# Kernel tuning notes

Measured on AMD Instinct MI355X. Metric: run time of the kernel, lower is better.

The kernel has to match this reference:

```python
import jax, jax.numpy as jnp
import numpy as np

NEG = 0.2  # LeakyReLU slope

def lrelu(x):
    return jnp.where(x >= 0, x, NEG * x)

def conv2d(x, w, pad):
    return jax.lax.conv_general_dilated(x, w, (1, 1), [(pad, pad), (pad, pad)],
                                        dimension_numbers=('NCHW', 'OIHW', 'NCHW'))

def maxpool2(x):
    return jax.lax.reduce_window(x, -jnp.inf, jax.lax.max, (1, 1, 2, 2), (1, 1, 2, 2), 'VALID')

def batchnorm(x, g, b, eps=1e-5):
    m = jnp.mean(x, axis=(0, 2, 3), keepdims=True)
    v = jnp.var(x, axis=(0, 2, 3), keepdims=True)
    return (x - m) / jnp.sqrt(v + eps) * g[None, :, None, None] + b[None, :, None, None]

def features(x, cw1, bg1, bb1, cw2, bg2, bb2, cw3, bg3, bb3, cw4, bg4, bb4):
    x = maxpool2(lrelu(batchnorm(conv2d(x, cw1, 1), bg1, bb1)))
    x = maxpool2(lrelu(batchnorm(conv2d(x, cw2, 1), bg2, bb2)))
    x = lrelu(batchnorm(conv2d(x, cw3, 1), bg3, bb3))
    x = lrelu(batchnorm(conv2d(x, cw4, 1), bg4, bb4))
    return x  # [B,64,16,16]

def mhsa(x, wq, bq, wk, bk, wv, bv, rel_h, rel_w, ln_g, ln_b, heads=4):
    B, C, W, H = x.shape
    d, hw = C // heads, W * H
    def proj(w, b):
        return (jnp.einsum('oc,bchw->bohw', w, x) + b[None, :, None, None]).reshape(B, heads, d, hw)
    q, k, v = proj(wq, bq), proj(wk, bk), proj(wv, bv)
    cc = jnp.einsum('bhdi,bhdj->bhij', q, k)                 # content-content
    pos = (rel_h + rel_w).reshape(heads, d, hw)              # relative position bias
    cp = jnp.einsum('hdi,bhdj->bhij', pos, q)                # content-position
    attn = jax.nn.softmax(cc + cp, axis=-1)
    out = jnp.einsum('bhdj,bhij->bhdi', v, attn).reshape(B, C, W, H)
    m = jnp.mean(out, axis=(1, 2, 3), keepdims=True)
    va = jnp.var(out, axis=(1, 2, 3), keepdims=True)
    out = (out - m) / jnp.sqrt(va + 1e-5) * ln_g[None] + ln_b[None]
    return out + x

def cbam(x, cw1, cb1, cw2, cb2, sw, sb):
    avg, mx = jnp.mean(x, axis=(2, 3)), jnp.max(x, axis=(2, 3))
    def exc(f):
        return jnp.einsum('oc,bc->bo', cw2, jax.nn.relu(jnp.einsum('oc,bc->bo', cw1, f) + cb1)) + cb2
    x = jax.nn.sigmoid(exc(avg) + exc(mx))[:, :, None, None] * x
    sf = jnp.stack([jnp.mean(x, axis=1), jnp.max(x, axis=1)], axis=1)  # [B,2,H,W]
    sa = jax.nn.sigmoid(conv2d(sf, sw, 3) + sb[None, :, None, None])
    return sa * x

def sa_module(x, mh, cb):
    return mhsa(x, *mh) + cbam(x, *cb) + x

def setup_inputs() -> dict:
    key = jax.random.key(0)
    ks = jax.random.split(key, 24)
    rn = lambda k, s, sc=1.0: jax.random.normal(k, s, dtype=jnp.float32) * sc
    inp = {
        'input1': rn(ks[0], (64, 1, 64, 64)),
        'input2': rn(ks[1], (5, 5, 1, 64, 64)),
        'conv1_w': rn(ks[2], (64, 1, 3, 3), 0.3),
        'bn1_g': jnp.ones(64), 'bn1_b': jnp.zeros(64),
        'conv2_w': rn(ks[3], (64, 64, 3, 3), 0.05),
        'bn2_g': jnp.ones(64), 'bn2_b': jnp.zeros(64),
        'conv3_w': rn(ks[4], (64, 64, 3, 3), 0.05),
        'bn3_g': jnp.ones(64), 'bn3_b': jnp.zeros(64),
        'conv4_w': rn(ks[5], (64, 64, 3, 3), 0.05),
        'bn4_g': jnp.ones(64), 'bn4_b': jnp.zeros(64),
        'wq': rn(ks[6], (64, 64), 0.12), 'bq': rn(ks[7], (64,), 0.01),
        'wk': rn(ks[8], (64, 64), 0.12), 'bk': rn(ks[9], (64,), 0.01),
        'wv': rn(ks[10], (64, 64), 0.12), 'bv': rn(ks[11], (64,), 0.01),
        'rel_h': rn(ks[12], (1, 4, 16, 1, 16)),
        'rel_w': rn(ks[13], (1, 4, 16, 16, 1)),
        'ln_g': jnp.ones((64, 16, 16)), 'ln_b': jnp.zeros((64, 16, 16)),
        'ca_w1': rn(ks[14], (4, 64), 0.15), 'ca_b1': jnp.zeros(4),
        'ca_w2': rn(ks[15], (64, 4), 0.15), 'ca_b2': jnp.zeros(64),
        'sa_w': rn(ks[16], (1, 2, 7, 7), 0.1), 'sa_b': jnp.zeros(1),
        'cls_w': rn(ks[17], (256,), 0.05),
    }
    return inp

def reference(input1, input2, conv1_w, bn1_g, bn1_b, conv2_w, bn2_g, bn2_b,
              conv3_w, bn3_g, bn3_b, conv4_w, bn4_g, bn4_b,
              wq, bq, wk, bk, wv, bv, rel_h, rel_w, ln_g, ln_b,
              ca_w1, ca_b1, ca_w2, ca_b2, sa_w, sa_b, cls_w):
    fa = (conv1_w, bn1_g, bn1_b, conv2_w, bn2_g, bn2_b, conv3_w, bn3_g, bn3_b, conv4_w, bn4_g, bn4_b)
    mh = (wq, bq, wk, bk, wv, bv, rel_h, rel_w, ln_g, ln_b)
    cb = (ca_w1, ca_b1, ca_w2, ca_b2, sa_w, sa_b)
    q = sa_module(features(input1, *fa), mh, cb)                      # [B,64,16,16]
    S = jax.vmap(lambda imgs: sa_module(features(imgs, *fa), mh, cb))(input2)  # [ncls,shot,64,16,16]
    ncls, shot = input2.shape[0], input2.shape[1]
    B, C, Hh, Ww = q.shape
    hw = Hh * Ww
    # per-class covariance over channels (CovaBlock.cal_covariance)
    X = S.transpose(0, 2, 1, 3, 4).reshape(ncls, C, shot * hw)
    Xc = X - jnp.mean(X, axis=2, keepdims=True)
    cov = jnp.einsum('ncm,ndm->ncd', Xc, Xc) / (hw * shot - 1)        # [ncls,C,C]
    # query similarity: diag(q^T Cov q) done as fused quadratic form
    Q = q.reshape(B, C, hw)
    Qn = Q / jnp.linalg.norm(Q, axis=2, keepdims=True)
    sim = jnp.einsum('bci,jcd,bdi->bji', Qn, cov, Qn)                 # [B,ncls,hw]
    # classifier: LeakyReLU -> Dropout(eval=identity) -> Conv1d(k=hw, stride=hw, no bias)
    out = jnp.einsum('bjk,k->bj', lrelu(sim), cls_w)
    return out
```

## Files before the change

kernel.cpp:

```cpp
#include <hip/hip_runtime.h>
#include <hip/hip_bf16.h>

__device__ __forceinline__ float lrelu(float x){ return x >= 0.f ? x : 0.2f*x; }
__device__ __forceinline__ float sigm(float x){ return 1.f/(1.f+__expf(-x)); }

typedef short short8 __attribute__((ext_vector_type(8)));
typedef float f32x16 __attribute__((ext_vector_type(16)));

static constexpr size_t OFF_X0    = 0;
static constexpr size_t OFF_POS   = 475712;
static constexpr size_t OFF_WQT   = 492096;
static constexpr size_t OFF_STATS = 504384;
static constexpr size_t OFF_P1    = 507456;
static constexpr size_t OFF_P2    = 7092224;
static constexpr size_t OFF_S3    = 8937728;
static constexpr size_t OFF_S4    = 8943872;
static constexpr size_t OFF_WH3   = 8950016;
static constexpr size_t OFF_WL3   = 8968448;
static constexpr size_t OFF_WH4   = 8986880;
static constexpr size_t OFF_WL4   = 9005312;
static constexpr size_t OFF_RES   = 10714688;
static constexpr size_t OFF_MU    = 12172864;
static constexpr size_t OFF_COV   = 12173184;
static constexpr size_t OFF_SIM   = 12193664;
static constexpr size_t OFF_R1    = 12275584;
static constexpr size_t OFF_C2    = OFF_R1;
static constexpr size_t OFF_ATP   = OFF_R1;
static constexpr size_t OFF_C3    = OFF_R1 + 5832704;
static constexpr size_t OFF_C4    = OFF_R1 + 8749056;
static constexpr size_t OFF_CKV   = OFF_R1 + 10207232;
static constexpr size_t OFF_C3P   = OFF_R1 + 10207232;
static constexpr size_t OFF_MHRAW = OFF_R1 + 14581760;
static constexpr size_t OFF_QN    = OFF_R1 + 17543680;
static constexpr size_t OFF_WH    = OFF_R1 + 21737984;
static constexpr size_t OFF_WL    = OFF_WH + 18432;

__device__ __forceinline__ int bn_group(int img){ return (img < 64) ? 0 : (1 + (img-64)/5); }

__device__ __forceinline__ void bn_ab(const float* __restrict__ sums, int g, int c, float n,
                                      float gw, float bw, float& a, float& b)
{
    const float sum = sums[(g*64+c)*2], ss = sums[(g*64+c)*2+1];
    const float m = sum/n;
    const float var = fmaxf(ss/n - m*m, 0.f);
    const float istd = 1.f/sqrtf(var + 1e-5f);
    a = gw*istd;
    b = bw - m*a;
}

__device__ __forceinline__ void bn_ab_s8(const float* __restrict__ sums, int g, int c, float n,
                                         float gw, float bw, float& a, float& b)
{
    float sum = 0.f, ss = 0.f;
#pragma unroll
    for (int s=0;s<8;s++){
        sum += sums[s*768 + (g*64+c)*2];
        ss  += sums[s*768 + (g*64+c)*2 + 1];
    }
    const float m = sum/n;
    const float var = fmaxf(ss/n - m*m, 0.f);
    const float istd = 1.f/sqrtf(var + 1e-5f);
    a = gw*istd;
    b = bw - m*a;
}

__global__ __launch_bounds__(256) void prep_k(const float* __restrict__ in1, const float* __restrict__ in2,
        const float* __restrict__ relh, const float* __restrict__ relw,
        const float* __restrict__ wq, const float* __restrict__ wk, const float* __restrict__ wv,
        const float* __restrict__ cw2, const float* __restrict__ cw3, const float* __restrict__ cw4,
        float* __restrict__ ws)
{
    int idx = blockIdx.x*256 + threadIdx.x;
    if (idx < 364544) { ws[OFF_X0+idx] = (idx < 262144 ? in1[idx] : in2[idx-262144]); return; }
    idx -= 364544;
    if (idx < 16384) {
        const int h = idx>>12, r = idx&4095, i = r>>4, d = r&15;
        ws[OFF_POS+idx] = relh[h*256 + d*16 + (i&15)] + relw[h*256 + d*16 + (i>>4)];
        return;
    }
    idx -= 16384;
    if (idx < 12288) {
        const int s = idx/4096, r = idx%4096, c = r>>6, o = r&63;
        const float* wp = (s==0)?wq:((s==1)?wk:wv);
        ws[OFF_WQT+idx] = wp[o*64 + c];
        return;
    }
    idx -= 12288;
    if (idx < 3072) { ws[OFF_STATS+idx] = 0.f; return; }
    idx -= 3072;
    if (idx < 20480) { ws[OFF_COV+idx] = 0.f; return; }
    idx -= 20480;
    if (idx < 12288) { ws[OFF_S3+idx] = 0.f; return; }
    idx -= 12288;
    if (idx < 110592) {
        const int which = idx / 36864, r0 = idx - which*36864;
        const int och = r0/576, rr = r0%576, cin = rr/9, k9 = rr%9;
        const float* cwp = (which==0)?cw2:((which==1)?cw3:cw4);
        const float v = cwp[r0];
        __hip_bfloat16 hb = __float2bfloat16(v);
        const float hv = __bfloat162float(hb);
        __hip_bfloat16 lb = __float2bfloat16(v - hv);
        const size_t oh = (which==0)?OFF_WH:((which==1)?OFF_WH3:OFF_WH4);
        const size_t ol = (which==0)?OFF_WL:((which==1)?OFF_WL3:OFF_WL4);
        unsigned short* WH = (unsigned short*)(ws + oh);
        unsigned short* WL = (unsigned short*)(ws + ol);
        const int d = k9*4096 + och*64 + cin;
        WH[d] = *(unsigned short*)&hb;
        WL[d] = *(unsigned short*)&lb;
        return;
    }
    idx -= 110592;
    if (idx < 751872) {
        const int img = idx/8448, r = idx%8448;
        const int pos = r>>6, d = r&63;
        int ypad, xpad;
        if (pos < 68){ ypad = (pos<34)?0:33; xpad = (pos<34)?pos:(pos-34); }
        else { const int q = pos-68; ypad = 1 + (q>>1); xpad = (q&1)*33; }
        ws[OFF_P1 + (((size_t)img*34 + ypad)*34 + xpad)*64 + d] = 0.f;
        return;
    }
    idx -= 751872;
    if (idx < 387328) {
        const int img = idx/4352, r = idx%4352;
        const int pos = r>>6, d = r&63;
        int ypad, xpad;
        if (pos < 36){ ypad = (pos<18)?0:17; xpad = (pos<18)?pos:(pos-18); }
        else { const int q = pos-36; ypad = 1 + (q>>1); xpad = (q&1)*17; }
        ws[OFF_P2 + (((size_t)img*18 + ypad)*18 + xpad)*64 + d] = 0.f;
        return;
    }
    idx -= 387328;
    if (idx < 387328) {
        const int img = idx/4352, r = idx%4352;
        const int pos = r>>6, d = r&63;
        int ypad, xpad;
        if (pos < 36){ ypad = (pos<18)?0:17; xpad = (pos<18)?pos:(pos-18); }
        else { const int q = pos-36; ypad = 1 + (q>>1); xpad = (q&1)*17; }
        ws[OFF_C3P + (((size_t)img*18 + ypad)*18 + xpad)*64 + d] = 0.f;
    }
}

template<int H, int W, int CIN, int CH, int OCB, int PT, bool STORE, bool INBN>
__global__ __launch_bounds__(256) void conv3x3_k(const float* __restrict__ in,
                                                 const float* __restrict__ wt,
                                                 float* __restrict__ out,
                                                 float* __restrict__ bnsum,
// ... 152 lines not shown
    }
    const int g = bn_group(img);
    const float n = (float)(((g==0)?64:5) * 4096);
    __syncthreads();
    const int p = t>>1, half = t&1;
    const int ly = p>>5, ox = p&31;
    float r[4][4];
#pragma unroll
    for (int dy=0;dy<4;dy++){
        const float* Lr = xl + (2*ly+dy)*64;
#pragma unroll
        for (int dx=0;dx<4;dx++){
            const int xx = 2*ox-1+dx;
            r[dy][dx] = (xx>=0 && xx<64) ? Lr[xx] : 0.f;
        }
    }
    short8 hv[4], lv[4];
#pragma unroll
    for (int o=0;o<32;o++){
        const int och = half*32 + o;
        float w[9];
#pragma unroll
        for (int k=0;k<9;k++) w[k] = cw[och*9+k];
        float a, b;
        bn_ab(sums, g, och, n, gw[och], bw[och], a, b);
        float best = -1e30f;
#pragma unroll
        for (int sy=0;sy<2;sy++)
#pragma unroll
          for (int sx=0;sx<2;sx++){
            float s=0.f;
#pragma unroll
            for (int ky=0;ky<3;ky++)
#pragma unroll
              for (int kx=0;kx<3;kx++) s += r[sy+ky][sx+kx]*w[ky*3+kx];
            best = fmaxf(best, lrelu(a*s+b));
          }
        __hip_bfloat16 hb = __float2bfloat16(best);
        const float hf = __bfloat162float(hb);
        __hip_bfloat16 lb = __float2bfloat16(best - hf);
        hv[o>>3][o&7] = (short)*(unsigned short*)&hb;
        lv[o>>3][o&7] = (short)*(unsigned short*)&lb;
    }
    const size_t base = ((((size_t)img*34 + (oy0+ly) + 1)*34) + ox + 1)*128 + half*32;
#pragma unroll
    for (int j=0;j<4;j++){
        *(short8*)(p1p + base + j*8)      = hv[j];
        *(short8*)(p1p + base + 64 + j*8) = lv[j];
    }
}

__global__ __launch_bounds__(256) void conv2mfma_k(const unsigned short* __restrict__ p1p,
        const unsigned short* __restrict__ whi, const unsigned short* __restrict__ wlo,
        float* __restrict__ c2)
{
    __shared__ __align__(16) unsigned short Bx[136*128];
    const int img = blockIdx.x, rowblk = blockIdx.y;
    const int t = threadIdx.x;
    {
        const unsigned short* src = p1p + (((size_t)img*34 + rowblk*2)*34)*128;
        for (int idx=t; idx<2176; idx+=256){
            const int pos = idx>>4, sub = idx&15;
            const short8 v = *(const short8*)(src + pos*128 + sub*8);
            *(short8*)(Bx + pos*128 + ((sub ^ (pos&7))<<3)) = v;
        }
    }
    __syncthreads();
    const int lane = t & 63, wv = t >> 6;
    const int mt = wv & 1, ntp = wv >> 1;
    const int m = lane & 31, kg = lane >> 5;
    f32x16 acc;
#pragma unroll
    for (int r=0;r<16;r++) acc[r]=0.f;

#pragma unroll
    for (int ky=0; ky<3; ky++){
#pragma unroll
      for (int kx=0; kx<3; kx++){
        const int s = ky*3 + kx;
        const unsigned short* wh = whi + ((s*64 + mt*32 + m)<<6) + kg*8;
        const unsigned short* wl = wlo + ((s*64 + mt*32 + m)<<6) + kg*8;
        const int pos = (ntp+ky)*34 + m + kx;
        const int pb  = pos << 7;
        const int sw  = (pos & 7) << 3;
#pragma unroll
        for (int ch=0; ch<4; ch++){
            const short8 ah = *(const short8*)(wh + ch*16);
            const short8 al = *(const short8*)(wl + ch*16);
            const short8 bh = *(const short8*)(Bx + pb + ((ch*16 + (kg<<3)) ^ sw));
            const short8 bl = *(const short8*)(Bx + pb + (64 + ((ch*16 + (kg<<3)) ^ sw)));
            acc = __builtin_amdgcn_mfma_f32_32x32x16_bf16(ah, bh, acc, 0,0,0);
            acc = __builtin_amdgcn_mfma_f32_32x32x16_bf16(al, bh, acc, 0,0,0);
            acc = __builtin_amdgcn_mfma_f32_32x32x16_bf16(ah, bl, acc, 0,0,0);
        }
      }
    }
    const int py = rowblk*2 + ntp;
    float* co = c2 + ((size_t)img*64)*1024 + py*32 + m;
#pragma unroll
    for (int r=0; r<16; r++){
        const int och = mt*32 + (r&3) + 8*(r>>2) + 4*kg;
        co[(size_t)och*1024] = acc[r];
    }
}

__global__ __launch_bounds__(256) void bnstats2_k(const float* __restrict__ in, float* __restrict__ sums)
{
    __shared__ float rs[4], rq[4];
    const int img = blockIdx.x, c = blockIdx.y, t = threadIdx.x;
    const float4 v = ((const float4*)(in + ((size_t)img*64 + c)*1024))[t];
    float s = v.x+v.y+v.z+v.w;
    float q = v.x*v.x+v.y*v.y+v.z*v.z+v.w*v.w;
#pragma unroll
    for (int off=32; off>0; off>>=1){ s += __shfl_xor(s, off); q += __shfl_xor(q, off); }
    if ((t&63)==0){ rs[t>>6]=s; rq[t>>6]=q; }
    __syncthreads();
    if (t==0){
        const int g = bn_group(img);
        atomicAdd(&sums[(g*64+c)*2],   rs[0]+rs[1]+rs[2]+rs[3]);
        atomicAdd(&sums[(g*64+c)*2+1], rq[0]+rq[1]+rq[2]+rq[3]);
    }
}

__global__ __launch_bounds__(256) void bnpool_pack_k(const float* __restrict__ c2,
        const float* __restrict__ sums, const float* __restrict__ gw, const float* __restrict__ bw,
        unsigned short* __restrict__ p2p)
{
    __shared__ float aA[64], aB[64];
    const int img = blockIdx.x, cb = blockIdx.y, t = threadIdx.x;
    const int g = bn_group(img);
    if (t < 64){
        const float n = (float)(((g==0)?64:5) * 1024);
        float a, b;
        bn_ab(sums, g, t, n, gw[t], bw[t], a, b);
        aA[t]=a; aB[t]=b;
    }
    __syncthreads();
    const int oy = t>>4, ox = t&15;
    const float* pim = c2 + (size_t)img*65536 + (size_t)cb*32768 + oy*64 + ox*2;
    short8 hv[4], lv[4];
#pragma unroll
    for (int j8=0;j8<4;j8++){
#pragma unroll
      for (int e=0;e<8;e++){
        const int j = j8*8 + e;
        const int c = cb*32 + j;
        const float* pl = pim + (size_t)j*1024;
        const float2 u = *(const float2*)pl;
        const float2 v = *(const float2*)(pl + 32);
        const float a = aA[c], b = aB[c];
        const float best = fmaxf(fmaxf(lrelu(a*u.x+b), lrelu(a*u.y+b)),
                                 fmaxf(lrelu(a*v.x+b), lrelu(a*v.y+b)));
        __hip_bfloat16 hb = __float2bfloat16(best);
        const float hf = __bfloat162float(hb);
        __hip_bfloat16 lb = __float2bfloat16(best - hf);
        hv[j8][e] = (short)*(unsigned short*)&hb;
        lv[j8][e] = (short)*(unsigned short*)&lb;
      }
    }
    unsigned short* dst = p2p + (((size_t)img*18 + oy+1)*18 + ox+1)*128 + cb*32;
#pragma unroll
    for (int j=0;j<4;j++){
        *(short8*)(dst + j*8)      = hv[j];
        *(short8*)(dst + 64 + j*8) = lv[j];
    }
}

__global__ __launch_bounds__(256) void conv16mfma_k(const unsigned short* __restrict__ pack,
        const unsigned short* __restrict__ whi, const unsigned short* __restrict__ wlo,
        float* __restrict__ out, float* __restrict__ bnsum)
{
    __shared__ __align__(16) unsigned short Bx[108*128];
    const int img = blockIdx.x, rowblk = blockIdx.y;
    const int t = threadIdx.x;
    {
        const unsigned short* src = pack + (((size_t)img*18 + rowblk*4)*18)*128;
        for (int idx=t; idx<1728; idx+=256){
            const int pos = idx>>4, sub = idx&15;
            const short8 v = *(const short8*)(src + pos*128 + sub*8);
            *(short8*)(Bx + pos*128 + ((sub ^ (pos&7))<<3)) = v;
        }
    }
    __syncthreads();
    const int lane = t & 63, wv = t >> 6;
    const int mt = wv & 1, np = wv >> 1;
    const int m = lane & 31, kg = lane >> 5;
    f32x16 acc;
#pragma unroll
    for (int r=0;r<16;r++) acc[r]=0.f;

#pragma unroll
    for (int ky=0; ky<3; ky++){
#pragma unroll
      for (int kx=0; kx<3; kx++){
        const int s = ky*3 + kx;
        const unsigned short* wh = whi + ((s*64 + mt*32 + m)<<6) + kg*8;
        const unsigned short* wl = wlo + ((s*64 + mt*32 + m)<<6) + kg*8;
        const int pos = (np*2 + (m>>4) + ky)*18 + (m&15) + kx;
        const int pb  = pos << 7;
        const int sw  = (pos & 7) << 3;
#pragma unroll
        for (int ch=0; ch<4; ch++){
            const short8 ah = *(const short8*)(wh + ch*16);
            const short8 al = *(const short8*)(wl + ch*16);
            const short8 bh = *(const short8*)(Bx + pb + ((ch*16 + (kg<<3)) ^ sw));
            const short8 bl = *(const short8*)(Bx + pb + (64 + ((ch*16 + (kg<<3)) ^ sw)));
            acc = __builtin_amdgcn_mfma_f32_32x32x16_bf16(ah, bh, acc, 0,0,0);
            acc = __builtin_amdgcn_mfma_f32_32x32x16_bf16(al, bh, acc, 0,0,0);
            acc = __builtin_amdgcn_mfma_f32_32x32x16_bf16(ah, bl, acc, 0,0,0);
        }
      }
    }
    float* co = out + (size_t)img*16384 + rowblk*64 + np*32 + m;
#pragma unroll
    for (int r=0; r<16; r++){
        const int och = mt*32 + (r&3) + 8*(r>>2) + 4*kg;
        co[(size_t)och*256] = acc[r];
    }
    const int g = bn_group(img);
    float* bs = bnsum + (rowblk*2 + np)*768;
#pragma unroll
    for (int r=0; r<16; r++){
        float sv = acc[r], qv = acc[r]*acc[r];
#pragma unroll
        for (int off=16; off>0; off>>=1){ sv += __shfl_xor(sv, off); qv += __shfl_xor(qv, off); }
        if (m == r){
            const int och = mt*32 + (r&3) + 8*(r>>2) + 4*kg;
            atomicAdd(&bs[(g*64+och)*2],   sv);
            atomicAdd(&bs[(g*64+och)*2+1], qv);
        }
    }
}

__global__ __launch_bounds__(256) void c3pack_k(const float* __restrict__ c3,
        const float* __restrict__ s3, const float* __restrict__ gw, const float* __restrict__ bw,
        unsigned short* __restrict__ c3p)
{
    __shared__ float aA[64], aB[64];
    const int img = blockIdx.x, cb = blockIdx.y, t = threadIdx.x;
    const int g = bn_group(img);
    if (t < 64){
        const float n = (float)(((g==0)?64:5) * 256);
        float a, b;
        bn_ab_s8(s3, g, t, n, gw[t], bw[t], a, b);
        aA[t]=a; aB[t]=b;
    }
    __syncthreads();
    const float* pim = c3 + (size_t)img*16384 + (size_t)cb*8192 + t;
    short8 hv[4], lv[4];
#pragma unroll
    for (int j8=0;j8<4;j8++){
#pragma unroll
      for (int e=0;e<8;e++){
        const int j = j8*8 + e;
        const int c = cb*32 + j;
        const float v = lrelu(aA[c]*pim[(size_t)j*256] + aB[c]);
        __hip_bfloat16 hb = __float2bfloat16(v);
        const float hf = __bfloat162float(hb);
        __hip_bfloat16 lb = __float2bfloat16(v - hf);
// ... 62 lines not shown
        const float4 v = make_float4(acc[0][ii],acc[1][ii],acc[2][ii],acc[3][ii]);
        *(float4*)(ckv + (((size_t)img*4 + h)*256 + i0+ii)*48 + sofs + d0) = v;
    }
}

__global__ __launch_bounds__(256) void attnp_k(const float* __restrict__ ckv, const float* __restrict__ pos,
                               float* __restrict__ part)
{
    const int img = blockIdx.x, h = blockIdx.y, jc = blockIdx.z, i = threadIdx.x;
    const size_t jb = (((size_t)img*4 + h)*256)*48;
    float areg[32];
    {
        const float* myrow = ckv + jb + (size_t)i*48;
#pragma unroll
        for (int k=0;k<4;k++) *(float4*)&areg[4*k]    = *(const float4*)(myrow + 16 + 4*k);
#pragma unroll
        for (int k=0;k<4;k++) *(float4*)&areg[16+4*k] = *(const float4*)(pos + h*4096 + i*16 + 4*k);
    }
    float mrun = -1e30f, l = 0.f;
    float accv[16];
#pragma unroll
    for (int d=0;d<16;d++) accv[d]=0.f;

    const int jend = jc*64 + 64;
    for (int j0=jc*64; j0<jend; j0+=2){
        const float* r0 = ckv + jb + (size_t)j0*48;
        const float* r1 = r0 + 48;
        float s0a=0.f, s0b=0.f, s1a=0.f, s1b=0.f;
#pragma unroll
        for (int dd=0; dd<16; ++dd){
            s0a += areg[2*dd]  *r0[2*dd];
            s0b += areg[2*dd+1]*r0[2*dd+1];
            s1a += areg[2*dd]  *r1[2*dd];
            s1b += areg[2*dd+1]*r1[2*dd+1];
        }
        const float s0 = s0a+s0b, s1 = s1a+s1b;
        const float mnew = fmaxf(mrun, fmaxf(s0,s1));
        const float al = __expf(mrun - mnew);
        const float e0 = __expf(s0 - mnew), e1 = __expf(s1 - mnew);
        mrun = mnew;
        l = l*al + e0 + e1;
        const float* v0 = r0 + 32;
        const float* v1 = r1 + 32;
#pragma unroll
        for (int d=0;d<16;d++) accv[d] = accv[d]*al + e0*v0[d] + e1*v1[d];
    }
    float* pp = part + ((((size_t)img*4 + h)*4 + jc)*18)*256;
    pp[i]       = mrun;
    pp[256 + i] = l;
#pragma unroll
    for (int d=0;d<16;d++) pp[(2+d)*256 + i] = accv[d];
}

__global__ __launch_bounds__(256) void attnm_k(const float* __restrict__ part, float* __restrict__ mhraw)
{
    const int img = blockIdx.x, h = blockIdx.y, i = threadIdx.x;
    const float* pb = part + (((size_t)img*4 + h)*4*18)*256;
    float mc[4], lc[4];
#pragma unroll
    for (int c=0;c<4;c++){ mc[c] = pb[c*4608 + i]; lc[c] = pb[c*4608 + 256 + i]; }
    const float ms = fmaxf(fmaxf(mc[0],mc[1]), fmaxf(mc[2],mc[3]));
    float wgt[4]; float ls = 0.f;
#pragma unroll
    for (int c=0;c<4;c++){ wgt[c] = __expf(mc[c]-ms); ls += wgt[c]*lc[c]; }
    const float rl = 1.f/ls;
#pragma unroll
    for (int d=0;d<16;d++){
        float v = 0.f;
#pragma unroll
        for (int c=0;c<4;c++) v += wgt[c]*pb[c*4608 + (2+d)*256 + i];
        mhraw[((size_t)img*64 + h*16 + d)*256 + i] = v*rl;
    }
}

__global__ __launch_bounds__(256) void post_k(const float* __restrict__ mhraw,
        const float* __restrict__ lng, const float* __restrict__ lnb,
        const float* __restrict__ c4,
        const float* __restrict__ sums4, const float* __restrict__ gw4, const float* __restrict__ bw4,
        const float* __restrict__ w1, const float* __restrict__ b1,
        const float* __restrict__ w2, const float* __restrict__ b2,
        const float* __restrict__ sw, const float* __restrict__ sb,
        float* __restrict__ res)
{
    __shared__ float r1[256], r2[256];
    __shared__ float favg[64], fmx[64], z1s[8], ca[64];
    __shared__ float sf[512];
    __shared__ float wl[98];
    __shared__ float mh_s[2];
    __shared__ float aA[64], aB[64];
    __shared__ float sa_l[256];
    const int img = blockIdx.x, t = threadIdx.x;
    const float* mb  = mhraw + (size_t)img*16384;
    const float* fbr = c4    + (size_t)img*16384;

    if (t<64){
        const int gi = bn_group(img);
        const float nin = (float)(((gi==0)?64:5) * 256);
        float a, b;
        bn_ab_s8(sums4, gi, t, nin, gw4[t], bw4[t], a, b);
        aA[t]=a; aB[t]=b;
    }
    if (t<98) wl[t] = sw[t];

    {
        const float4* mb4 = (const float4*)mb;
        float s=0.f, ss=0.f;
        for (int i=t; i<4096; i+=256){
            const float4 v = mb4[i];
            s  += v.x+v.y+v.z+v.w;
            ss += v.x*v.x+v.y*v.y+v.z*v.z+v.w*v.w;
        }
        r1[t]=s; r2[t]=ss; __syncthreads();
        for (int st=128;st>0;st>>=1){ if(t<st){r1[t]+=r1[t+st]; r2[t]+=r2[t+st];} __syncthreads(); }
        if (t==0){
            const float m = r1[0]/16384.f;
            const float var = fmaxf(r2[0]/16384.f - m*m, 0.f);
            mh_s[0]=m; mh_s[1]=1.f/sqrtf(var+1e-5f);
        }
    }
    {
        const int c = t>>2, part = t&3;
        const float a = aA[c], b = aB[c];
        const float4* p4 = (const float4*)(fbr + c*256 + part*64);
        float s=0.f, mx=-1e30f;
        for (int k=0;k<16;k++){
            const float4 v = p4[k];
            const float f0=lrelu(a*v.x+b), f1=lrelu(a*v.y+b), f2=lrelu(a*v.z+b), f3=lrelu(a*v.w+b);
            s += f0+f1+f2+f3;
            mx = fmaxf(mx, fmaxf(fmaxf(f0,f1),fmaxf(f2,f3)));
        }
        __syncthreads();
        r1[t]=s; r2[t]=mx;
        __syncthreads();
        if (t<64){
            favg[t] = (r1[t*4]+r1[t*4+1]+r1[t*4+2]+r1[t*4+3])/256.f;
            fmx[t]  = fmaxf(fmaxf(r2[t*4],r2[t*4+1]),fmaxf(r2[t*4+2],r2[t*4+3]));
        }
    }
    __syncthreads();
    if (t<8){
        const int which = t>>2, o = t&3;
        const float* f = which? fmx : favg;
        float z = b1[o];
        for (int c=0;c<64;c++) z += w1[o*64+c]*f[c];
        z1s[t] = fmaxf(z, 0.f);
    }
    __syncthreads();
    if (t<64){
        float z = 2.f*b2[t];
#pragma unroll
        for (int k=0;k<4;k++) z += w2[t*4+k]*(z1s[k]+z1s[4+k]);
        ca[t] = sigm(z);
    }
    __syncthreads();
    {
        float s=0.f, mx=-1e30f;
        for (int c=0;c<64;c++){
            const float fv = lrelu(aA[c]*fbr[c*256+t] + aB[c]);
            const float v = ca[c]*fv;
            s += v; mx = fmaxf(mx, v);
        }
        sf[t]     = s/64.f;
        sf[256+t] = mx;
    }
    __syncthreads();
    {
        float sacc = sb[0];
        const int y = t>>4, x = t&15;
        for (int ch=0; ch<2; ++ch)
          for (int ky=0; ky<7; ++ky){
            const int yy = y+ky-3;
            if (yy<0||yy>=16) continue;
            for (int kx=0; kx<7; ++kx){
                const int xx = x+kx-3;
                if (xx<0||xx>=16) continue;
                sacc += sf[ch*256 + yy*16 + xx]*wl[ch*49 + ky*7 + kx];
            }
          }
        sa_l[t] = sigm(sacc);
    }
    __syncthreads();
    {
        const int q = t & 63;
        const int cb = t >> 6;
        const float m = mh_s[0], istd = mh_s[1];
        const float4* mb4 = (const float4*)mb;
        const float4* fb4 = (const float4*)fbr;
        const float4* lg4 = (const float4*)lng;
        const float4* lb4 = (const float4*)lnb;
        float4* res4 = (float4*)(res + (size_t)img*16384);
        const float sa0=sa_l[4*q], sa1=sa_l[4*q+1], sa2=sa_l[4*q+2], sa3=sa_l[4*q+3];
#pragma unroll 4
        for (int cc=0; cc<16; ++cc){
            const int c = cb*16 + cc;
            const int i4 = c*64 + q;
            const float4 mv = mb4[i4], fv = fb4[i4], gv = lg4[i4], bv = lb4[i4];
            const float a = aA[c], b = aB[c], cf = ca[c];
            float4 r;
            r.x = (mv.x-m)*istd*gv.x + bv.x + lrelu(a*fv.x+b)*(2.f + sa0*cf);
            r.y = (mv.y-m)*istd*gv.y + bv.y + lrelu(a*fv.y+b)*(2.f + sa1*cf);
            r.z = (mv.z-m)*istd*gv.z + bv.z + lrelu(a*fv.z+b)*(2.f + sa2*cf);
            r.w = (mv.w-m)*istd*gv.w + bv.w + lrelu(a*fv.w+b)*(2.f + sa3*cf);
            res4[i4] = r;
        }
    }
}

__global__ __launch_bounds__(256) void covmu_k(const float* __restrict__ res, float* __restrict__ mu)
{
    __shared__ float r1[256];
    const int n = blockIdx.x, c = blockIdx.y, t = threadIdx.x;
    float s=0.f;
    for (int sh=0; sh<5; ++sh)
        s += res[((size_t)(64 + n*5 + sh)*64 + c)*256 + t];
    r1[t]=s; __syncthreads();
    for (int st=128;st>0;st>>=1){ if(t<st) r1[t]+=r1[t+st]; __syncthreads(); }
    if (t==0) mu[n*64+c] = r1[0]/1280.f;
}

__global__ __launch_bounds__(256) void cov_k(const float* __restrict__ res, const float* __restrict__ mu,
                                             float* __restrict__ cov)
{
    __shared__ float Xl[64*129];
    const int n = blockIdx.x, by = blockIdx.y, sh = blockIdx.z, t = threadIdx.x;
    const int c = by*16 + (t>>4);
    const int d0 = (t&15)*4;
    float acc[4] = {0.f,0.f,0.f,0.f};
    for (int half=0; half<2; ++half){
        __syncthreads();
        for (int idx=t; idx<8192; idx+=256){
            const int ch = idx>>7, p = idx&127;
            Xl[ch*129+p] = res[((size_t)(64+n*5+sh)*64 + ch)*256 + half*128 + p] - mu[n*64+ch];
        }
        __syncthreads();
        for (int p=0;p<128;p++){
            const float xc = Xl[c*129+p];
#pragma unroll
            for (int k=0;k<4;k++) acc[k] += xc*Xl[(d0+k)*129+p];
        }
    }
#pragma unroll
    for (int k=0;k<4;k++) atomicAdd(&cov[((size_t)n*64 + c)*64 + d0+k], acc[k]*(1.f/1279.f));
}

__global__ __launch_bounds__(64) void qn_k(const float* __restrict__ res, float* __restrict__ qn)
{
    const int b = blockIdx.x, c = blockIdx.y, t = threadIdx.x;
    const size_t base = ((size_t)b*64 + c)*256;
    const float4 v = *(const float4*)(res + base + t*4);
// ... 41 lines not shown
                pt[cc][2] += cw[cc]*vv.z;
                pt[cc][3] += cw[cc]*vv.w;
            }
        }
#pragma unroll
        for (int ii=0;ii<4;ii++){
            float s = 0.f;
#pragma unroll
            for (int cc=0;cc<4;cc++) s += pt[cc][ii]*Vl[(c0+cc)*68 + i0+ii];
            atomicAdd(&simred[j*64 + i0 + ii], s);
        }
    }
    __syncthreads();
    for (int idx=t; idx<320; idx+=256){
        const int j = idx>>6, il = idx&63;
        sim[((size_t)b*5 + j)*256 + i0g + il] = simred[idx];
    }
}

__global__ __launch_bounds__(256) void cls_k(const float* __restrict__ sim, const float* __restrict__ cw,
                                             float* __restrict__ out)
{
    __shared__ float red[256];
    const int b = blockIdx.x, t = threadIdx.x;
    const float w = cw[t];
    for (int j=0;j<5;j++){
        const float v = sim[((size_t)b*5 + j)*256 + t];
        red[t] = lrelu(v)*w;
        __syncthreads();
        for (int st=128;st>0;st>>=1){ if(t<st) red[t]+=red[t+st]; __syncthreads(); }
        if (t==0) out[b*5+j] = red[0];
        __syncthreads();
    }
}

extern "C" void kernel_launch(void* const* d_in, const int* in_sizes, int n_in,
                              void* d_out, int out_size, void* d_ws, size_t ws_size,
                              hipStream_t stream)
{
    const float* IN[31];
    for (int i=0;i<31;i++) IN[i] = (const float*)d_in[i];
    float* W = (float*)d_ws;
    float* OUT = (float*)d_out;
    const unsigned short* WHp  = (const unsigned short*)(W + OFF_WH);
    const unsigned short* WLp  = (const unsigned short*)(W + OFF_WL);
    const unsigned short* WH3p = (const unsigned short*)(W + OFF_WH3);
    const unsigned short* WL3p = (const unsigned short*)(W + OFF_WL3);
    const unsigned short* WH4p = (const unsigned short*)(W + OFF_WH4);
    const unsigned short* WL4p = (const unsigned short*)(W + OFF_WL4);
    unsigned short* P1P = (unsigned short*)(W + OFF_P1);
    unsigned short* P2P = (unsigned short*)(W + OFF_P2);
    unsigned short* C3P = (unsigned short*)(W + OFF_C3P);

    prep_k<<<8072,256,0,stream>>>(IN[0],IN[1],IN[20],IN[21],IN[14],IN[16],IN[18],
                                  IN[5],IN[8],IN[11],W);

    conv3x3_k<64,64,1,1,4,4,false,false><<<dim3(89,16),256,0,stream>>>(W+OFF_X0, IN[2], nullptr, W+OFF_STATS, nullptr,nullptr,nullptr,0);
    bnpoolconv1_k<<<dim3(89,8),256,0,stream>>>(W+OFF_X0, IN[2], W+OFF_STATS, IN[3], IN[4], P1P);

    conv2mfma_k<<<dim3(89,16),256,0,stream>>>(P1P, WHp, WLp, W+OFF_C2);
    bnstats2_k<<<dim3(89,64),256,0,stream>>>(W+OFF_C2, W+OFF_STATS+768);
    bnpool_pack_k<<<dim3(89,2),256,0,stream>>>(W+OFF_C2, W+OFF_STATS+768, IN[6], IN[7], P2P);

    conv16mfma_k<<<dim3(89,4),256,0,stream>>>(P2P, WH3p, WL3p, W+OFF_C3, W+OFF_S3);
    c3pack_k<<<dim3(89,2),256,0,stream>>>(W+OFF_C3, W+OFF_S3, IN[9], IN[10], C3P);

    conv16mfma_k<<<dim3(89,4),256,0,stream>>>(C3P, WH4p, WL4p, W+OFF_C4, W+OFF_S4);

    proj_k<<<dim3(89,3),256,0,stream>>>(W+OFF_C4, W+OFF_WQT, IN[15], IN[17], IN[19],
                                        W+OFF_S4, IN[12], IN[13], W+OFF_CKV);
    attnp_k<<<dim3(89,4,4),256,0,stream>>>(W+OFF_CKV, W+OFF_POS, W+OFF_ATP);
    attnm_k<<<dim3(89,4),256,0,stream>>>(W+OFF_ATP, W+OFF_MHRAW);

    post_k<<<89,256,0,stream>>>(W+OFF_MHRAW, IN[22], IN[23], W+OFF_C4,
                                W+OFF_S4, IN[12], IN[13],
                                IN[24], IN[25], IN[26], IN[27], IN[28], IN[29], W+OFF_RES);

    covmu_k<<<dim3(5,64),256,0,stream>>>(W+OFF_RES, W+OFF_MU);
    cov_k<<<dim3(5,4,5),256,0,stream>>>(W+OFF_RES, W+OFF_MU, W+OFF_COV);
    qn_k<<<dim3(64,64),64,0,stream>>>(W+OFF_RES, W+OFF_QN);
    sim_k<<<dim3(64,4),256,0,stream>>>(W+OFF_QN, W+OFF_COV, W+OFF_SIM);
    cls_k<<<64,256,0,stream>>>(W+OFF_SIM, IN[30], OUT);
}
```

Baseline: 527.6 us.

## Fuse conv2 BN statistics into MFMA conv and double per-block row tile

Removes the separate bnstats2 kernel by computing per-channel sum and sum-of-squares in the conv2 MFMA epilogue, using shuffles and atomics into 16 partial slots that are zeroed in prep. Each conv2 block now covers four output rows, with two accumulators per wave that share the weight fragments, so weight loads are reused and the grid is halved. The LDS swizzle is widened to 16 positions in both conv kernels to reduce bank conflicts. This saves a full re-read of the conv2 output and one launch, at the cost of more LDS and registers per block and contended atomics.

```diff
diff --git a/kernel.cpp b/kernel.cpp
--- a/kernel.cpp
+++ b/kernel.cpp
@@ -19,6 +19,7 @@
 static constexpr size_t OFF_WL3   = 8968448;
 static constexpr size_t OFF_WH4   = 8986880;
 static constexpr size_t OFF_WL4   = 9005312;
+static constexpr size_t OFF_S2    = 9023744;
 static constexpr size_t OFF_RES   = 10714688;
 static constexpr size_t OFF_MU    = 12172864;
 static constexpr size_t OFF_COV   = 12173184;
@@ -64,6 +65,22 @@
     b = bw - m*a;
 }
 
+__device__ __forceinline__ void bn_ab_s16(const float* __restrict__ sums, int g, int c, float n,
+                                          float gw, float bw, float& a, float& b)
+{
+    float sum = 0.f, ss = 0.f;
+#pragma unroll
+    for (int s=0;s<16;s++){
+        sum += sums[s*768 + (g*64+c)*2];
+        ss  += sums[s*768 + (g*64+c)*2 + 1];
+    }
+    const float m = sum/n;
+    const float var = fmaxf(ss/n - m*m, 0.f);
+    const float istd = 1.f/sqrtf(var + 1e-5f);
+    a = gw*istd;
+    b = bw - m*a;
+}
+
 __global__ __launch_bounds__(256) void prep_k(const float* __restrict__ in1, const float* __restrict__ in2,
         const float* __restrict__ relh, const float* __restrict__ relw,
         const float* __restrict__ wq, const float* __restrict__ wk, const float* __restrict__ wv,
@@ -91,6 +108,8 @@
     if (idx < 20480) { ws[OFF_COV+idx] = 0.f; return; }
     idx -= 20480;
     if (idx < 12288) { ws[OFF_S3+idx] = 0.f; return; }
+    idx -= 12288;
+    if (idx < 12288) { ws[OFF_S2+idx] = 0.f; return; }
     idx -= 12288;
     if (idx < 110592) {
         const int which = idx / 36864, r0 = idx - which*36864;
@@ -350,26 +369,26 @@
 
 __global__ __launch_bounds__(256) void conv2mfma_k(const unsigned short* __restrict__ p1p,
         const unsigned short* __restrict__ whi, const unsigned short* __restrict__ wlo,
-        float* __restrict__ c2)
-{
-    __shared__ __align__(16) unsigned short Bx[136*128];
+        float* __restrict__ c2, float* __restrict__ bnsum)
+{
+    __shared__ __align__(16) unsigned short Bx[204*128];
     const int img = blockIdx.x, rowblk = blockIdx.y;
     const int t = threadIdx.x;
     {
-        const unsigned short* src = p1p + (((size_t)img*34 + rowblk*2)*34)*128;
-        for (int idx=t; idx<2176; idx+=256){
+        const unsigned short* src = p1p + (((size_t)img*34 + rowblk*4)*34)*128;
+        for (int idx=t; idx<3264; idx+=256){
             const int pos = idx>>4, sub = idx&15;
             const short8 v = *(const short8*)(src + pos*128 + sub*8);
-            *(short8*)(Bx + pos*128 + ((sub ^ (pos&7))<<3)) = v;
+            *(short8*)(Bx + pos*128 + ((sub ^ (pos&15))<<3)) = v;
         }
     }
     __syncthreads();
     const int lane = t & 63, wv = t >> 6;
     const int mt = wv & 1, ntp = wv >> 1;
     const int m = lane & 31, kg = lane >> 5;
-    f32x16 acc;
-#pragma unroll
-    for (int r=0;r<16;r++) acc[r]=0.f;
+    f32x16 acc0, acc1;
+#pragma unroll
+    for (int r=0;r<16;r++){ acc0[r]=0.f; acc1[r]=0.f; }
 
 #pragma unroll
     for (int ky=0; ky<3; ky++){
@@ -378,45 +397,53 @@
         const int s = ky*3 + kx;
         const unsigned short* wh = whi + ((s*64 + mt*32 + m)<<6) + kg*8;
         const unsigned short* wl = wlo + ((s*64 + mt*32 + m)<<6) + kg*8;
-        const int pos = (ntp+ky)*34 + m + kx;
-        const int pb  = pos << 7;
-        const int sw  = (pos & 7) << 3;
+        const int pos0 = (ntp*2 + ky)*34 + m + kx;
+        const int pos1 = pos0 + 34;
+        const int pb0 = pos0 << 7, sw0 = (pos0 & 15) << 3;
+        const int pb1 = pos1 << 7, sw1 = (pos1 & 15) << 3;
+        short8 ah[4], al[4], b0h[4], b1h[4], b0l[4], b1l[4];
 #pragma unroll
         for (int ch=0; ch<4; ch++){
-            const short8 ah = *(const short8*)(wh + ch*16);
-            const short8 al = *(const short8*)(wl + ch*16);
-            const short8 bh = *(const short8*)(Bx + pb + ((ch*16 + (kg<<3)) ^ sw));
-            const short8 bl = *(const short8*)(Bx + pb + (64 + ((ch*16 + (kg<<3)) ^ sw)));
-            acc = __builtin_amdgcn_mfma_f32_32x32x16_bf16(ah, bh, acc, 0,0,0);
-            acc = __builtin_amdgcn_mfma_f32_32x32x16_bf16(al, bh, acc, 0,0,0);
-            acc = __builtin_amdgcn_mfma_f32_32x32x16_bf16(ah, bl, acc, 0,0,0);
+            const int o = ch*16 + (kg<<3);
+            ah[ch]  = *(const short8*)(wh + ch*16);
+            al[ch]  = *(const short8*)(wl + ch*16);
+            b0h[ch] = *(const short8*)(Bx + pb0 + (o ^ sw0));
+            b1h[ch] = *(const short8*)(Bx + pb1 + (o ^ sw1));
+            b0l[ch] = *(const short8*)(Bx + pb0 + ((64 + o) ^ sw0));
+            b1l[ch] = *(const short8*)(Bx + pb1 + ((64 + o) ^ sw1));
+        }
+#pragma unroll
+        for (int ch=0; ch<4; ch++){
+            acc0 = __builtin_amdgcn_mfma_f32_32x32x16_bf16(ah[ch], b0h[ch], acc0, 0,0,0);
+            acc1 = __builtin_amdgcn_mfma_f32_32x32x16_bf16(ah[ch], b1h[ch], acc1, 0,0,0);
+            acc0 = __builtin_amdgcn_mfma_f32_32x32x16_bf16(al[ch], b0h[ch], acc0, 0,0,0);
+            acc1 = __builtin_amdgcn_mfma_f32_32x32x16_bf16(al[ch], b1h[ch], acc1, 0,0,0);
+            acc0 = __builtin_amdgcn_mfma_f32_32x32x16_bf16(ah[ch], b0l[ch], acc0, 0,0,0);
+            acc1 = __builtin_amdgcn_mfma_f32_32x32x16_bf16(ah[ch], b1l[ch], acc1, 0,0,0);
         }
       }
     }
-    const int py = rowblk*2 + ntp;
-    float* co = c2 + ((size_t)img*64)*1024 + py*32 + m;
+    const int pr0 = rowblk*4 + ntp*2;
+    float* co = c2 + (size_t)img*65536 + (size_t)pr0*32 + m;
 #pragma unroll
     for (int r=0; r<16; r++){
         const int och = mt*32 + (r&3) + 8*(r>>2) + 4*kg;
-        co[(size_t)och*1024] = acc[r];
-    }
-}
-
-__global__ __launch_bounds__(256) void bnstats2_k(const float* __restrict__ in, float* __restrict__ sums)
-{
-    __shared__ float rs[4], rq[4];
-    const int img = blockIdx.x, c = blockIdx.y, t = threadIdx.x;
-    const float4 v = ((const float4*)(in + ((size_t)img*64 + c)*1024))[t];
-    float s = v.x+v.y+v.z+v.w;
-    float q = v.x*v.x+v.y*v.y+v.z*v.z+v.w*v.w;
-#pragma unroll
-    for (int off=32; off>0; off>>=1){ s += __shfl_xor(s, off); q += __shfl_xor(q, off); }
-    if ((t&63)==0){ rs[t>>6]=s; rq[t>>6]=q; }
-    __syncthreads();
-    if (t==0){
-        const int g = bn_group(img);
-        atomicAdd(&sums[(g*64+c)*2],   rs[0]+rs[1]+rs[2]+rs[3]);
-        atomicAdd(&sums[(g*64+c)*2+1], rq[0]+rq[1]+rq[2]+rq[3]);
+        co[(size_t)och*1024]      = acc0[r];
+        co[(size_t)och*1024 + 32] = acc1[r];
+    }
+    const int g = bn_group(img);
+    float* bs = bnsum + (rowblk*2 + ntp)*768;
+#pragma unroll
+    for (int r=0; r<16; r++){
+        float sv = acc0[r] + acc1[r];
+        float qv = acc0[r]*acc0[r] + acc1[r]*acc1[r];
+#pragma unroll
+        for (int off=16; off>0; off>>=1){ sv += __shfl_xor(sv, off); qv += __shfl_xor(qv, off); }
+        if (m == r){
+            const int och = mt*32 + (r&3) + 8*(r>>2) + 4*kg;
+            atomicAdd(&bs[(g*64+och)*2],   sv);
+            atomicAdd(&bs[(g*64+och)*2+1], qv);
+        }
     }
 }
 
@@ -430,7 +457,7 @@
     if (t < 64){
         const float n = (float)(((g==0)?64:5) * 1024);
         float a, b;
-        bn_ab(sums, g, t, n, gw[t], bw[t], a, b);
+        bn_ab_s16(sums, g, t, n, gw[t], bw[t], a, b);
         aA[t]=a; aB[t]=b;
     }
     __syncthreads();
@@ -476,7 +503,7 @@
         for (int idx=t; idx<1728; idx+=256){
             const int pos = idx>>4, sub = idx&15;
             const short8 v = *(const short8*)(src + pos*128 + sub*8);
-            *(short8*)(Bx + pos*128 + ((sub ^ (pos&7))<<3)) = v;
+            *(short8*)(Bx + pos*128 + ((sub ^ (pos&15))<<3)) = v;
         }
     }
     __syncthreads();
@@ -496,13 +523,14 @@
         const unsigned short* wl = wlo + ((s*64 + mt*32 + m)<<6) + kg*8;
         const int pos = (np*2 + (m>>4) + ky)*18 + (m&15) + kx;
         const int pb  = pos << 7;
-        const int sw  = (pos & 7) << 3;
+        const int sw  = (pos & 15) << 3;
 #pragma unroll
         for (int ch=0; ch<4; ch++){
+            const int o = ch*16 + (kg<<3);
             const short8 ah = *(const short8*)(wh + ch*16);
             const short8 al = *(const short8*)(wl + ch*16);
-            const short8 bh = *(const short8*)(Bx + pb + ((ch*16 + (kg<<3)) ^ sw));
-            const short8 bl = *(const short8*)(Bx + pb + (64 + ((ch*16 + (kg<<3)) ^ sw)));
+            const short8 bh = *(const short8*)(Bx + pb + (o ^ sw));
+            const short8 bl = *(const short8*)(Bx + pb + ((64 + o) ^ sw));
             acc = __builtin_amdgcn_mfma_f32_32x32x16_bf16(ah, bh, acc, 0,0,0);
             acc = __builtin_amdgcn_mfma_f32_32x32x16_bf16(al, bh, acc, 0,0,0);
             acc = __builtin_amdgcn_mfma_f32_32x32x16_bf16(ah, bl, acc, 0,0,0);
@@ -961,15 +989,14 @@
     unsigned short* P2P = (unsigned short*)(W + OFF_P2);
     unsigned short* C3P = (unsigned short*)(W + OFF_C3P);
 
-    prep_k<<<8072,256,0,stream>>>(IN[0],IN[1],IN[20],IN[21],IN[14],IN[16],IN[18],
+    prep_k<<<8119,256,0,stream>>>(IN[0],IN[1],IN[20],IN[21],IN[14],IN[16],IN[18],
                                   IN[5],IN[8],IN[11],W);
 
     conv3x3_k<64,64,1,1,4,4,false,false><<<dim3(89,16),256,0,stream>>>(W+OFF_X0, IN[2], nullptr, W+OFF_STATS, nullptr,nullptr,nullptr,0);
     bnpoolconv1_k<<<dim3(89,8),256,0,stream>>>(W+OFF_X0, IN[2], W+OFF_STATS, IN[3], IN[4], P1P);
 
-    conv2mfma_k<<<dim3(89,16),256,0,stream>>>(P1P, WHp, WLp, W+OFF_C2);
-    bnstats2_k<<<dim3(89,64),256,0,stream>>>(W+OFF_C2, W+OFF_STATS+768);
-    bnpool_pack_k<<<dim3(89,2),256,0,stream>>>(W+OFF_C2, W+OFF_STATS+768, IN[6], IN[7], P2P);
+    conv2mfma_k<<<dim3(89,8),256,0,stream>>>(P1P, WHp, WLp, W+OFF_C2, W+OFF_S2);
+    bnpool_pack_k<<<dim3(89,2),256,0,stream>>>(W+OFF_C2, W+OFF_S2, IN[6], IN[7], P2P);
 
     conv16mfma_k<<<dim3(89,4),256,0,stream>>>(P2P, WH3p, WL3p, W+OFF_C3, W+OFF_S3);
     c3pack_k<<<dim3(89,2),256,0,stream>>>(W+OFF_C3, W+OFF_S3, IN[9], IN[10], C3P);
```

After: 500.9 us. 1.05x faster.

## Fuse attention merge into post kernel and widen LDS swizzle in MFMA convs

Applied to the files above, without the earlier changes.

Removes the separate attnm_k kernel. post_k now merges the four partial softmax chunks per head itself and holds the attention output in a 64KB shared buffer, which avoids a global round trip of the MHSA output and one launch. The conv MFMA kernels change their LDS XOR swizzle from 8 to 16 positions to cut bank conflicts. BN2 stats move to their own zeroed buffer. The large shared array in post_k lowers occupancy, though that kernel runs only 89 blocks anyway.

```diff
diff --git a/kernel.cpp b/kernel.cpp
--- a/kernel.cpp
+++ b/kernel.cpp
@@ -19,6 +19,7 @@
 static constexpr size_t OFF_WL3   = 8968448;
 static constexpr size_t OFF_WH4   = 8986880;
 static constexpr size_t OFF_WL4   = 9005312;
+static constexpr size_t OFF_S2    = 9023744;
 static constexpr size_t OFF_RES   = 10714688;
 static constexpr size_t OFF_MU    = 12172864;
 static constexpr size_t OFF_COV   = 12173184;
@@ -30,7 +31,6 @@
 static constexpr size_t OFF_C4    = OFF_R1 + 8749056;
 static constexpr size_t OFF_CKV   = OFF_R1 + 10207232;
 static constexpr size_t OFF_C3P   = OFF_R1 + 10207232;
-static constexpr size_t OFF_MHRAW = OFF_R1 + 14581760;
 static constexpr size_t OFF_QN    = OFF_R1 + 17543680;
 static constexpr size_t OFF_WH    = OFF_R1 + 21737984;
 static constexpr size_t OFF_WL    = OFF_WH + 18432;
@@ -92,6 +92,8 @@
     idx -= 20480;
     if (idx < 12288) { ws[OFF_S3+idx] = 0.f; return; }
     idx -= 12288;
+    if (idx < 768) { ws[OFF_S2+idx] = 0.f; return; }
+    idx -= 768;
     if (idx < 110592) {
         const int which = idx / 36864, r0 = idx - which*36864;
         const int och = r0/576, rr = r0%576, cin = rr/9, k9 = rr%9;
@@ -360,7 +362,7 @@
         for (int idx=t; idx<2176; idx+=256){
             const int pos = idx>>4, sub = idx&15;
             const short8 v = *(const short8*)(src + pos*128 + sub*8);
-            *(short8*)(Bx + pos*128 + ((sub ^ (pos&7))<<3)) = v;
+            *(short8*)(Bx + pos*128 + ((sub ^ (pos&15))<<3)) = v;
         }
     }
     __syncthreads();
@@ -380,13 +382,14 @@
         const unsigned short* wl = wlo + ((s*64 + mt*32 + m)<<6) + kg*8;
         const int pos = (ntp+ky)*34 + m + kx;
         const int pb  = pos << 7;
-        const int sw  = (pos & 7) << 3;
+        const int sw  = (pos & 15) << 3;
 #pragma unroll
         for (int ch=0; ch<4; ch++){
+            const int o = ch*16 + (kg<<3);
             const short8 ah = *(const short8*)(wh + ch*16);
             const short8 al = *(const short8*)(wl + ch*16);
-            const short8 bh = *(const short8*)(Bx + pb + ((ch*16 + (kg<<3)) ^ sw));
-            const short8 bl = *(const short8*)(Bx + pb + (64 + ((ch*16 + (kg<<3)) ^ sw)));
+            const short8 bh = *(const short8*)(Bx + pb + (o ^ sw));
+            const short8 bl = *(const short8*)(Bx + pb + ((64 + o) ^ sw));
             acc = __builtin_amdgcn_mfma_f32_32x32x16_bf16(ah, bh, acc, 0,0,0);
             acc = __builtin_amdgcn_mfma_f32_32x32x16_bf16(al, bh, acc, 0,0,0);
             acc = __builtin_amdgcn_mfma_f32_32x32x16_bf16(ah, bl, acc, 0,0,0);
@@ -394,7 +397,7 @@
       }
     }
     const int py = rowblk*2 + ntp;
-    float* co = c2 + ((size_t)img*64)*1024 + py*32 + m;
+    float* co = c2 + (size_t)img*65536 + py*32 + m;
 #pragma unroll
     for (int r=0; r<16; r++){
         const int och = mt*32 + (r&3) + 8*(r>>2) + 4*kg;
@@ -476,7 +479,7 @@
         for (int idx=t; idx<1728; idx+=256){
             const int pos = idx>>4, sub = idx&15;
             const short8 v = *(const short8*)(src + pos*128 + sub*8);
-            *(short8*)(Bx + pos*128 + ((sub ^ (pos&7))<<3)) = v;
+            *(short8*)(Bx + pos*128 + ((sub ^ (pos&15))<<3)) = v;
         }
     }
     __syncthreads();
@@ -496,13 +499,14 @@
         const unsigned short* wl = wlo + ((s*64 + mt*32 + m)<<6) + kg*8;
         const int pos = (np*2 + (m>>4) + ky)*18 + (m&15) + kx;
         const int pb  = pos << 7;
-        const int sw  = (pos & 7) << 3;
+        const int sw  = (pos & 15) << 3;
 #pragma unroll
         for (int ch=0; ch<4; ch++){
+            const int o = ch*16 + (kg<<3);
             const short8 ah = *(const short8*)(wh + ch*16);
             const short8 al = *(const short8*)(wl + ch*16);
-            const short8 bh = *(const short8*)(Bx + pb + ((ch*16 + (kg<<3)) ^ sw));
-            const short8 bl = *(const short8*)(Bx + pb + (64 + ((ch*16 + (kg<<3)) ^ sw)));
+            const short8 bh = *(const short8*)(Bx + pb + (o ^ sw));
+            const short8 bl = *(const short8*)(Bx + pb + ((64 + o) ^ sw));
             acc = __builtin_amdgcn_mfma_f32_32x32x16_bf16(ah, bh, acc, 0,0,0);
             acc = __builtin_amdgcn_mfma_f32_32x32x16_bf16(al, bh, acc, 0,0,0);
             acc = __builtin_amdgcn_mfma_f32_32x32x16_bf16(ah, bl, acc, 0,0,0);
@@ -671,28 +675,7 @@
     for (int d=0;d<16;d++) pp[(2+d)*256 + i] = accv[d];
 }
 
-__global__ __launch_bounds__(256) void attnm_k(const float* __restrict__ part, float* __restrict__ mhraw)
-{
-    const int img = blockIdx.x, h = blockIdx.y, i = threadIdx.x;
-    const float* pb = part + (((size_t)img*4 + h)*4*18)*256;
-    float mc[4], lc[4];
-#pragma unroll
-    for (int c=0;c<4;c++){ mc[c] = pb[c*4608 + i]; lc[c] = pb[c*4608 + 256 + i]; }
-    const float ms = fmaxf(fmaxf(mc[0],mc[1]), fmaxf(mc[2],mc[3]));
-    float wgt[4]; float ls = 0.f;
-#pragma unroll
-    for (int c=0;c<4;c++){ wgt[c] = __expf(mc[c]-ms); ls += wgt[c]*lc[c]; }
-    const float rl = 1.f/ls;
-#pragma unroll
-    for (int d=0;d<16;d++){
-        float v = 0.f;
-#pragma unroll
-        for (int c=0;c<4;c++) v += wgt[c]*pb[c*4608 + (2+d)*256 + i];
-        mhraw[((size_t)img*64 + h*16 + d)*256 + i] = v*rl;
-    }
-}
-
-__global__ __launch_bounds__(256) void post_k(const float* __restrict__ mhraw,
+__global__ __launch_bounds__(256) void post_k(const float* __restrict__ part,
         const float* __restrict__ lng, const float* __restrict__ lnb,
         const float* __restrict__ c4,
         const float* __restrict__ sums4, const float* __restrict__ gw4, const float* __restrict__ bw4,
@@ -701,6 +684,7 @@
         const float* __restrict__ sw, const float* __restrict__ sb,
         float* __restrict__ res)
 {
+    __shared__ float mh_l[16384];
     __shared__ float r1[256], r2[256];
     __shared__ float favg[64], fmx[64], z1s[8], ca[64];
     __shared__ float sf[512];
@@ -709,8 +693,8 @@
     __shared__ float aA[64], aB[64];
     __shared__ float sa_l[256];
     const int img = blockIdx.x, t = threadIdx.x;
-    const float* mb  = mhraw + (size_t)img*16384;
-    const float* fbr = c4    + (size_t)img*16384;
+    const float* fbr = c4 + (size_t)img*16384;
+    const float* pb_img = part + (size_t)img*73728;
 
     if (t<64){
         const int gi = bn_group(img);
@@ -722,12 +706,28 @@
     if (t<98) wl[t] = sw[t];
 
     {
-        const float4* mb4 = (const float4*)mb;
+        float wgt[4][4], rl4[4];
+#pragma unroll
+        for (int h=0;h<4;h++){
+            const float* pbh = pb_img + h*18432;
+            float mc[4], lc[4];
+#pragma unroll
+            for (int c=0;c<4;c++){ mc[c] = pbh[c*4608 + t]; lc[c] = pbh[c*4608 + 256 + t]; }
+            const float ms = fmaxf(fmaxf(mc[0],mc[1]), fmaxf(mc[2],mc[3]));
+            float ls = 0.f;
+#pragma unroll
+            for (int c=0;c<4;c++){ wgt[h][c] = __expf(mc[c]-ms); ls += wgt[h][c]*lc[c]; }
+            rl4[h] = 1.f/ls;
+        }
         float s=0.f, ss=0.f;
-        for (int i=t; i<4096; i+=256){
-            const float4 v = mb4[i];
-            s  += v.x+v.y+v.z+v.w;
-            ss += v.x*v.x+v.y*v.y+v.z*v.z+v.w*v.w;
+#pragma unroll 4
+        for (int c=0;c<64;c++){
+            const int h = c>>4, d = c&15;
+            const float* pa = pb_img + h*18432 + (2+d)*256 + t;
+            const float v = (wgt[h][0]*pa[0] + wgt[h][1]*pa[4608]
+                           + wgt[h][2]*pa[9216] + wgt[h][3]*pa[13824]) * rl4[h];
+            mh_l[c*256 + t] = v;
+            s += v; ss += v*v;
         }
         r1[t]=s; r2[t]=ss; __syncthreads();
         for (int st=128;st>0;st>>=1){ if(t<st){r1[t]+=r1[t+st]; r2[t]+=r2[t+st];} __syncthreads(); }
@@ -738,9 +738,9 @@
         }
     }
     {
-        const int c = t>>2, part = t&3;
+        const int c = t>>2, part4 = t&3;
         const float a = aA[c], b = aB[c];
-        const float4* p4 = (const float4*)(fbr + c*256 + part*64);
+        const float4* p4 = (const float4*)(fbr + c*256 + part4*64);
         float s=0.f, mx=-1e30f;
         for (int k=0;k<16;k++){
             const float4 v = p4[k];
@@ -803,7 +803,6 @@
         const int q = t & 63;
         const int cb = t >> 6;
         const float m = mh_s[0], istd = mh_s[1];
-        const float4* mb4 = (const float4*)mb;
         const float4* fb4 = (const float4*)fbr;
         const float4* lg4 = (const float4*)lng;
         const float4* lb4 = (const float4*)lnb;
@@ -813,7 +812,8 @@
         for (int cc=0; cc<16; ++cc){
             const int c = cb*16 + cc;
             const int i4 = c*64 + q;
-            const float4 mv = mb4[i4], fv = fb4[i4], gv = lg4[i4], bv = lb4[i4];
+            const float4 mv = *(const float4*)&mh_l[c*256 + q*4];
+            const float4 fv = fb4[i4], gv = lg4[i4], bv = lb4[i4];
             const float a = aA[c], b = aB[c], cf = ca[c];
             float4 r;
             r.x = (mv.x-m)*istd*gv.x + bv.x + lrelu(a*fv.x+b)*(2.f + sa0*cf);
@@ -961,15 +961,15 @@
     unsigned short* P2P = (unsigned short*)(W + OFF_P2);
     unsigned short* C3P = (unsigned short*)(W + OFF_C3P);
 
-    prep_k<<<8072,256,0,stream>>>(IN[0],IN[1],IN[20],IN[21],IN[14],IN[16],IN[18],
+    prep_k<<<8074,256,0,stream>>>(IN[0],IN[1],IN[20],IN[21],IN[14],IN[16],IN[18],
                                   IN[5],IN[8],IN[11],W);
 
     conv3x3_k<64,64,1,1,4,4,false,false><<<dim3(89,16),256,0,stream>>>(W+OFF_X0, IN[2], nullptr, W+OFF_STATS, nullptr,nullptr,nullptr,0);
     bnpoolconv1_k<<<dim3(89,8),256,0,stream>>>(W+OFF_X0, IN[2], W+OFF_STATS, IN[3], IN[4], P1P);
 
     conv2mfma_k<<<dim3(89,16),256,0,stream>>>(P1P, WHp, WLp, W+OFF_C2);
-    bnstats2_k<<<dim3(89,64),256,0,stream>>>(W+OFF_C2, W+OFF_STATS+768);
-    bnpool_pack_k<<<dim3(89,2),256,0,stream>>>(W+OFF_C2, W+OFF_STATS+768, IN[6], IN[7], P2P);
+    bnstats2_k<<<dim3(89,64),256,0,stream>>>(W+OFF_C2, W+OFF_S2);
+    bnpool_pack_k<<<dim3(89,2),256,0,stream>>>(W+OFF_C2, W+OFF_S2, IN[6], IN[7], P2P);
 
     conv16mfma_k<<<dim3(89,4),256,0,stream>>>(P2P, WH3p, WL3p, W+OFF_C3, W+OFF_S3);
     c3pack_k<<<dim3(89,2),256,0,stream>>>(W+OFF_C3, W+OFF_S3, IN[9], IN[10], C3P);
@@ -979,9 +979,8 @@
     proj_k<<<dim3(89,3),256,0,stream>>>(W+OFF_C4, W+OFF_WQT, IN[15], IN[17], IN[19],
                                         W+OFF_S4, IN[12], IN[13], W+OFF_CKV);
     attnp_k<<<dim3(89,4,4),256,0,stream>>>(W+OFF_CKV, W+OFF_POS, W+OFF_ATP);
-    attnm_k<<<dim3(89,4),256,0,stream>>>(W+OFF_ATP, W+OFF_MHRAW);
-
-    post_k<<<89,256,0,stream>>>(W+OFF_MHRAW, IN[22], IN[23], W+OFF_C4,
+
+    post_k<<<89,256,0,stream>>>(W+OFF_ATP, IN[22], IN[23], W+OFF_C4,
                                 W+OFF_S4, IN[12], IN[13],
                                 IN[24], IN[25], IN[26], IN[27], IN[28], IN[29], W+OFF_RES);
 
```

Result: slower. 559.4 us (+6.0%).
